# Performance work log

Measured on AMD Instinct MI355X. Metric: run time of the kernel, lower is better.

The kernel has to match this reference:

```python
import jax, jax.numpy as jnp
import numpy as np

N_TX, N_USER, N_MERCH = 100000, 20000, 5000
E = 400000
F_IN, H, L = 32, 256, 2


def setup_inputs() -> dict:
    key = jax.random.key(0)
    ks = jax.random.split(key, 24)
    p = lambda k, s: 0.02 * jax.random.normal(k, s, dtype=jnp.float32)
    return {
        "x_tx": jax.random.normal(ks[0], (N_TX, F_IN), dtype=jnp.float32),
        "x_user": jax.random.normal(ks[1], (N_USER, H), dtype=jnp.float32),
        "x_merch": jax.random.normal(ks[2], (N_MERCH, H), dtype=jnp.float32),
        # input projection
        "Wp": p(ks[3], (F_IN, H)), "bp": jnp.zeros((H,), jnp.float32),
        # per-layer, per-edge-type SAGEConv params: lin_l (neighbor, with bias) and lin_r (root, no bias)
        "Wl": p(ks[4], (L, 4, H, H)), "bl": jnp.zeros((L, 4, H), jnp.float32),
        "Wr": p(ks[5], (L, 4, H, H)),
        # classifier head
        "Wc1": p(ks[6], (H, H // 2)), "bc1": jnp.zeros((H // 2,), jnp.float32),
        "Wc2": p(ks[7], (H // 2, 1)), "bc2": jnp.zeros((1,), jnp.float32),
        # revenue head
        "Wv1": p(ks[8], (H, H // 2)), "bv1": jnp.zeros((H // 2,), jnp.float32),
        "Wv2": p(ks[9], (H // 2, 1)), "bv2": jnp.zeros((1,), jnp.float32),
        # edge lists (src, dst) per relation
        "e_ut_src": jax.random.randint(ks[10], (E,), 0, N_USER, dtype=jnp.int32),
        "e_ut_dst": jax.random.randint(ks[11], (E,), 0, N_TX, dtype=jnp.int32),
        "e_tm_src": jax.random.randint(ks[12], (E,), 0, N_TX, dtype=jnp.int32),
        "e_tm_dst": jax.random.randint(ks[13], (E,), 0, N_MERCH, dtype=jnp.int32),
        "e_mt_src": jax.random.randint(ks[14], (E,), 0, N_MERCH, dtype=jnp.int32),
        "e_mt_dst": jax.random.randint(ks[15], (E,), 0, N_TX, dtype=jnp.int32),
        "e_tu_src": jax.random.randint(ks[16], (E,), 0, N_TX, dtype=jnp.int32),
        "e_tu_dst": jax.random.randint(ks[17], (E,), 0, N_USER, dtype=jnp.int32),
    }


def _seg_mean(x_src, src, dst, n_dst):
    # gather source features per edge, scatter-mean into destinations
    msg = x_src[src]                                        # [E, H]
    s = jax.ops.segment_sum(msg, dst, num_segments=n_dst)   # [n_dst, H]
    cnt = jax.ops.segment_sum(jnp.ones((dst.shape[0],), x_src.dtype), dst, num_segments=n_dst)
    return s / jnp.maximum(cnt, 1.0)[:, None]


def _sage(x_src, x_dst, src, dst, Wl, bl, Wr):
    # PyG SAGEConv: lin_l(mean_neighbors) + lin_r(x_dst)
    m = _seg_mean(x_src, src, dst, x_dst.shape[0])
    return m @ Wl + bl + x_dst @ Wr


def reference(x_tx, x_user, x_merch, Wp, bp, Wl, bl, Wr,
              Wc1, bc1, Wc2, bc2, Wv1, bv1, Wv2, bv2,
              e_ut_src, e_ut_dst, e_tm_src, e_tm_dst,
              e_mt_src, e_mt_dst, e_tu_src, e_tu_dst):
    xt = x_tx @ Wp + bp          # input_proj on 'transaction'
    xu, xm = x_user, x_merch     # already hidden_dim -> used as-is
    for l in range(L):
        t_from_u = _sage(xu, xt, e_ut_src, e_ut_dst, Wl[l, 0], bl[l, 0], Wr[l, 0])
        m_from_t = _sage(xt, xm, e_tm_src, e_tm_dst, Wl[l, 1], bl[l, 1], Wr[l, 1])
        t_from_m = _sage(xm, xt, e_mt_src, e_mt_dst, Wl[l, 2], bl[l, 2], Wr[l, 2])
        u_from_t = _sage(xt, xu, e_tu_src, e_tu_dst, Wl[l, 3], bl[l, 3], Wr[l, 3])
        # HeteroConv aggr='mean' over edge types per destination, then ReLU (dropout = identity in eval)
        xt = jax.nn.relu(0.5 * (t_from_u + t_from_m))
        xm = jax.nn.relu(m_from_t)
        xu = jax.nn.relu(u_from_t)
    fraud_logits = (jax.nn.relu(xt @ Wc1 + bc1) @ Wc2 + bc2)[:, 0]
    revenue_pred = (jax.nn.relu(xt @ Wv1 + bv1) @ Wv2 + bv2)[:, 0]
    return fraud_logits, revenue_pred
```

## Files before the change

kernel.cpp:

```cpp
#include <hip/hip_runtime.h>

#define NTX 100000
#define NUSER 20000
#define NMERCH 5000
#define HD 256
#define ROWPAD 128

using u16 = unsigned short;
typedef __attribute__((ext_vector_type(8))) short bf16x8;
typedef __attribute__((ext_vector_type(4))) float f32x4;

__device__ __forceinline__ u16 f2bf(float f){
  unsigned u = __float_as_uint(f);
  unsigned r = (u + 0x7FFFu + ((u >> 16) & 1u)) >> 16;
  return (u16)r;
}
__device__ __forceinline__ float bf2f(u16 b){
  return __uint_as_float(((unsigned)b) << 16);
}
__device__ __forceinline__ unsigned pk2(float a, float b){
  return (unsigned)f2bf(a) | ((unsigned)f2bf(b) << 16);
}

__device__ __forceinline__ void gather4(const u16* __restrict__ T, const int* __restrict__ ss,
    int j0, int j1, int lane, int c, float& o0, float& o1, float& o2, float& o3){
  float a0=0,a1=0,a2=0,a3=0, b0=0,b1=0,b2=0,b3=0;
  float c0=0,c1=0,c2=0,c3=0, d0=0,d1=0,d2=0,d3=0;
  for (int base = j0; base < j1; base += 64){
    int n = j1 - base; if (n > 64) n = 64;
    int idx = ss[base + (lane < n ? lane : 0)];
    for (int jj = 0; jj < n; jj += 4){
      int s0 = __shfl(idx, jj);
      int s1 = __shfl(idx, jj+1);
      int s2 = __shfl(idx, jj+2);
      int s3 = __shfl(idx, jj+3);
      ushort4 v0 = *(const ushort4*)(T + (size_t)s0*HD + c);
      ushort4 v1 = *(const ushort4*)(T + (size_t)s1*HD + c);
      ushort4 v2 = *(const ushort4*)(T + (size_t)s2*HD + c);
      ushort4 v3 = *(const ushort4*)(T + (size_t)s3*HD + c);
      a0 += bf2f(v0.x); a1 += bf2f(v0.y); a2 += bf2f(v0.z); a3 += bf2f(v0.w);
      if (jj+1 < n){ b0 += bf2f(v1.x); b1 += bf2f(v1.y); b2 += bf2f(v1.z); b3 += bf2f(v1.w); }
      if (jj+2 < n){ c0 += bf2f(v2.x); c1 += bf2f(v2.y); c2 += bf2f(v2.z); c3 += bf2f(v2.w); }
      if (jj+3 < n){ d0 += bf2f(v3.x); d1 += bf2f(v3.y); d2 += bf2f(v3.z); d3 += bf2f(v3.w); }
    }
  }
  o0 += (a0+b0)+(c0+d0); o1 += (a1+b1)+(c1+d1);
  o2 += (a2+b2)+(c2+d2); o3 += (a3+b3)+(c3+d3);
}

__device__ __forceinline__ int rel_n(int y){ return y==0?NTX: y==1?NMERCH: y==2?NTX:NUSER; }
__device__ __forceinline__ int rel_coff(int y){ return y==0?0: y==1?100000: y==2?105000:205000; }
__device__ __forceinline__ int rel_rpoff(int y){ return y==0?0: y==1?100001: y==2?105002:205003; }
__device__ __forceinline__ int rel_shift(int y){ return y==0?11: y==1?8: y==2?11:10; }
__device__ __forceinline__ int rel_np(int y){ return y==0?49: y==1?20: y==2?49:20; }
#define ECH 128
#define PSTW 72

__global__ __launch_bounds__(256) void csrA_kernel(const int* __restrict__ d0p, const int* __restrict__ d1p,
    const int* __restrict__ d2p, const int* __restrict__ d3p, int nE, int* __restrict__ PC){
  int y = blockIdx.y;
  const int* dst = y==0?d0p: y==1?d1p: y==2?d2p:d3p;
  int shift = rel_shift(y);
  __shared__ int cc[64];
  int t = threadIdx.x;
  if (t < 64) cc[t] = 0;
  __syncthreads();
  int CH = (nE + ECH - 1)/ECH;
  int e0 = blockIdx.x*CH, e1 = e0 + CH; if (e1 > nE) e1 = nE;
  for (int e = e0 + t*4; e < e1; e += 1024){
    int a = dst[e];
    int b = (e+1 < e1) ? dst[e+1] : -1;
    int c = (e+2 < e1) ? dst[e+2] : -1;
    int d = (e+3 < e1) ? dst[e+3] : -1;
    atomicAdd(&cc[a>>shift], 1);
    if (b >= 0) atomicAdd(&cc[b>>shift], 1);
    if (c >= 0) atomicAdd(&cc[c>>shift], 1);
    if (d >= 0) atomicAdd(&cc[d>>shift], 1);
  }
  __syncthreads();
  if (t < 64) PC[(((size_t)y*ECH + blockIdx.x)<<6) + t] = cc[t];
}

__global__ void csrB_kernel(int* __restrict__ PC, int* __restrict__ PST, int* __restrict__ RP, int nE){
  int y = blockIdx.y;
  int np = rel_np(y);
  int t = threadIdx.x;
  __shared__ int sh[64];
  int run = 0;
  if (t < np){
    for (int c = 0; c < ECH; ++c){
      size_t idx = (((size_t)y*ECH + c)<<6) + t;
      int v = PC[idx]; PC[idx] = run; run += v;
    }
  }
  sh[t] = run;
  __syncthreads();
  if (t == 0){
    int acc = 0;
    for (int i = 0; i < np; ++i){ int v = sh[i]; sh[i] = acc; acc += v; }
    PST[y*PSTW + np] = nE;
    RP[rel_rpoff(y) + rel_n(y)] = nE;
  }
  __syncthreads();
  if (t < np){
    int base = sh[t];
    PST[y*PSTW + t] = base;
    for (int c = 0; c < ECH; ++c){
      size_t idx = (((size_t)y*ECH + c)<<6) + t;
      PC[idx] += base;
    }
  }
}

__global__ __launch_bounds__(256) void csrC_kernel(
    const int* __restrict__ s0p, const int* __restrict__ d0p,
    const int* __restrict__ s1p, const int* __restrict__ d1p,
    const int* __restrict__ s2p, const int* __restrict__ d2p,
    const int* __restrict__ s3p, const int* __restrict__ d3p,
    const int* __restrict__ PC, int* __restrict__ EB, int nE){
  int y = blockIdx.y;
  const int* src = y==0?s0p: y==1?s1p: y==2?s2p:s3p;
  const int* dst = y==0?d0p: y==1?d1p: y==2?d2p:d3p;
  int shift = rel_shift(y);
  int mask = (1<<shift) - 1;
  __shared__ int cur[64];
  int t = threadIdx.x;
  if (t < 64) cur[t] = PC[(((size_t)y*ECH + blockIdx.x)<<6) + t];
  __syncthreads();
  int CH = (nE + ECH - 1)/ECH;
  int e0 = blockIdx.x*CH, e1 = e0 + CH; if (e1 > nE) e1 = nE;
  int* eb = EB + (size_t)y*nE;
  for (int e = e0 + t*4; e < e1; e += 1024){
    #pragma unroll
    for (int u = 0; u < 4; ++u){
      int ee = e + u;
      if (ee < e1){
        int d = dst[ee], s = src[ee];
        int pos = atomicAdd(&cur[d>>shift], 1);
        eb[pos] = ((d & mask) << 17) | s;
      }
    }
  }
}

__global__ __launch_bounds__(256) void csrD_kernel(const int* __restrict__ EB, const int* __restrict__ PST,
    int* __restrict__ RP, float* __restrict__ INV,
    int* __restrict__ ss0, int* __restrict__ ss1, int* __restrict__ ss2, int* __restrict__ ss3, int nE){
  int y = blockIdx.y;
  int np = rel_np(y);
  int part = blockIdx.x;
  if (part >= np) return;
  int shift = rel_shift(y);
  int n = rel_n(y);
  int gbase = part << shift;
  int len = n - gbase; int range = 1 << shift; if (len > range) len = range;
  __shared__ int cnt[2048];
  __shared__ int curs[2048];
  __shared__ int sh[256];
  int t = threadIdx.x;
  for (int i = t; i < len; i += 256) cnt[i] = 0;
  __syncthreads();
  const int* eb = EB + (size_t)y*nE;
  int j0 = PST[y*PSTW + part], j1 = PST[y*PSTW + part + 1];
  for (int j = j0 + t*4; j < j1; j += 1024){
    int a = eb[j];
    int b = (j+1 < j1) ? eb[j+1] : -1;
    int c = (j+2 < j1) ? eb[j+2] : -1;
    int d = (j+3 < j1) ? eb[j+3] : -1;
    atomicAdd(&cnt[a>>17], 1);
    if (b >= 0) atomicAdd(&cnt[b>>17], 1);
    if (c >= 0) atomicAdd(&cnt[c>>17], 1);
    if (d >= 0) atomicAdd(&cnt[d>>17], 1);
  }
  __syncthreads();
  int base8 = t*8;
  int vals[8]; int tsum = 0;
  #pragma unroll
  for (int u = 0; u < 8; ++u){
    int i = base8 + u;
    int v = (i < len) ? cnt[i] : 0;
    vals[u] = tsum; tsum += v;
  }
  sh[t] = tsum;
  __syncthreads();
  for (int o = 1; o < 256; o <<= 1){
    int v = (t >= o) ? sh[t-o] : 0;
    __syncthreads();
    sh[t] += v;
    __syncthreads();
  }
  int tbase = j0 + sh[t] - tsum;
  int rpo = rel_rpoff(y) + gbase;
  int ivo = rel_coff(y) + gbase;
  #pragma unroll
  for (int u = 0; u < 8; ++u){
    int i = base8 + u;
    if (i < len){
      int start = tbase + vals[u];
      curs[i] = start;
      RP[rpo + i] = start;
      INV[ivo + i] = 1.f/fmaxf((float)cnt[i], 1.f);
    }
  }
  __syncthreads();
  int* ss = y==0?ss0: y==1?ss1: y==2?ss2:ss3;
  for (int j = j0 + t*4; j < j1; j += 1024){
    #pragma unroll
    for (int u = 0; u < 4; ++u){
      int jj = j + u;
      if (jj < j1){
        int pk = eb[jj];
        int pos = atomicAdd(&curs[pk>>17], 1);
        ss[pos] = pk & 0x1FFFF;
      }
    }
  }
}

__global__ __launch_bounds__(256) void wprep_kernel(const float* __restrict__ Wl, const float* __restrict__ Wr,
    const float* __restrict__ Wp, const float* __restrict__ Wc1, const float* __restrict__ Wv1,
    const float* __restrict__ bc1, const float* __restrict__ bv1,
    u16* __restrict__ WTl, u16* __restrict__ WTr1, u16* __restrict__ WTr3, u16* __restrict__ WT02,
    u16* __restrict__ WTH, u16* __restrict__ WTp, float* __restrict__ bH){
  int y = blockIdx.y;
  int i = blockIdx.x*256 + threadIdx.x;
  if (y < 8){
    if (i < 65536){ int k=i>>8, n=i&255; WTl[(size_t)y*65536 + n*256 + k] = f2bf(Wl[(size_t)y*65536 + i]); }
  } else if (y < 10){
    int l = y-8;
    if (i < 65536){ int k=i>>8, n=i&255; WTr1[(size_t)l*65536 + n*256 + k] = f2bf(Wr[(size_t)(l*4+1)*65536 + i]); }
  } else if (y < 12){
    int l = y-10;
    if (i < 65536){ int k=i>>8, n=i&255; WTr3[(size_t)l*65536 + n*256 + k] = f2bf(Wr[(size_t)(l*4+3)*65536 + i]); }
  } else if (y < 14){
    int l = y-12;
    if (i < 65536){ int k=i>>8, n=i&255;
      WT02[(size_t)l*65536 + n*256 + k] = f2bf(Wr[(size_t)(l*4+0)*65536 + i] + Wr[(size_t)(l*4+2)*65536 + i]); }
  } else if (y == 14){
    if (i < 65536){ int k=i>>8, n=i&255;
      float v = (n < 128) ? Wc1[k*128 + n] : Wv1[k*128 + (n-128)];
      WTH[(size_t)n*256 + k] = f2bf(v); }
  } else {
    if (i < 8192){ int k=i>>8, n=i&255; WTp[(size_t)n*32 + k] = f2bf(Wp[i]); }
    if (i < 256) bH[i] = (i < 128) ? bc1[i] : bv1[i-128];
  }
}

__global__ __launch_bounds__(256) void cvt2_kernel(const float* __restrict__ xu,
    const float* __restrict__ xm, u16* __restrict__ XU, u16* __restrict__ XM){
  int y = blockIdx.y;
  const float* in = y==0?xu:xm;
  u16* out = y==0?XU:XM;
  int n4 = y==0?NUSER*HD/4:NMERCH*HD/4;
  int i = blockIdx.x*256 + threadIdx.x;
  if (i >= n4) return;
  float4 v = ((const float4*)in)[i];
  ushort4 o; o.x = f2bf(v.x); o.y = f2bf(v.y); o.z = f2bf(v.z); o.w = f2bf(v.w);
  ((ushort4*)out)[i] = o;
}

__global__ __launch_bounds__(256) void proj_gemm_kernel(const float* __restrict__ A, const u16* __restrict__ WT,
    const float* __restrict__ bias, u16* __restrict__ C, int M){
  __shared__ u16 As[128][40];
  __shared__ u16 Bs[128][40];
  int m0 = blockIdx.x * 128, n0 = blockIdx.y * 128;
  int t = threadIdx.x;
  int w = t >> 6, lane = t & 63;
  int wm = (w >> 1) << 6, wn = (w & 1) << 6;
  int lm = lane & 15;
  int lk = (lane >> 4) << 3;
  int sr = t >> 1, sc = (t & 1) << 4;
  float4 f0 = {0,0,0,0}, f1 = {0,0,0,0}, f2 = {0,0,0,0}, f3 = {0,0,0,0};
  if (m0 + sr < M){
    const float* ap = A + (size_t)(m0+sr)*32 + sc;
    f0 = *(const float4*)(ap+0); f1 = *(const float4*)(ap+4);
    f2 = *(const float4*)(ap+8); f3 = *(const float4*)(ap+12);
  }
  uint4 q0, q1;
  q0.x = pk2(f0.x,f0.y); q0.y = pk2(f0.z,f0.w); q0.z = pk2(f1.x,f1.y); q0.w = pk2(f1.z,f1.w);
  q1.x = pk2(f2.x,f2.y); q1.y = pk2(f2.z,f2.w); q1.z = pk2(f3.x,f3.y); q1.w = pk2(f3.z,f3.w);
  *(uint4*)&As[sr][sc] = q0;
  *(uint4*)&As[sr][sc+8] = q1;
  const u16* bp_ = WT + (size_t)(n0+sr)*32 + sc;
  *(uint4*)&Bs[sr][sc]   = *(const uint4*)(bp_);
  *(uint4*)&Bs[sr][sc+8] = *(const uint4*)(bp_ + 8);
  __syncthreads();
  bf16x8 af[4], bf[4];
  #pragma unroll
  for (int i = 0; i < 4; ++i) af[i] = *(const bf16x8*)&As[wm + i*16 + lm][lk];
  #pragma unroll
  for (int j = 0; j < 4; ++j) bf[j] = *(const bf16x8*)&Bs[wn + j*16 + lm][lk];
  f32x4 acc[4][4] = {};
  #pragma unroll
  for (int i = 0; i < 4; ++i)
    #pragma unroll
    for (int j = 0; j < 4; ++j)
      acc[i][j] = __builtin_amdgcn_mfma_f32_16x16x32_bf16(af[i], bf[j], acc[i][j], 0, 0, 0);
  int rsub = (lane >> 4) << 2;
  #pragma unroll
  for (int j = 0; j < 4; ++j){
    int col = n0 + wn + j*16 + lm;
    float bv = bias[col];
    #pragma unroll
    for (int i = 0; i < 4; ++i){
      int rbase = m0 + wm + i*16 + rsub;
      #pragma unroll
      for (int r = 0; r < 4; ++r){
        int row = rbase + r;
        if (row < M) C[(size_t)row*HD + col] = f2bf(acc[i][j][r] + bv);
      }
    }
  }
}

template<bool CBF, bool BIAS, bool RELU, bool ACCUM>
__global__ __launch_bounds__(256) void mfma_gemm_kernel(const u16* __restrict__ A, const u16* __restrict__ BT,
    const float* __restrict__ bias, const float* __restrict__ Cadd, void* __restrict__ Cp, int M, int K, int N){
  __shared__ u16 As[128][40];
  __shared__ u16 Bs[128][40];
  int m0 = blockIdx.x * 128, n0 = blockIdx.y * 128;
  int t = threadIdx.x;
  int w = t >> 6, lane = t & 63;
  int wm = (w >> 1) << 6, wn = (w & 1) << 6;
  int lm = lane & 15;
  int lk = (lane >> 4) << 3;
  f32x4 acc[4][4] = {};
  int sr0 = t >> 2, sk0 = (t & 3) << 3;
  int sr1 = sr0 + 64;
  for (int k0 = 0; k0 < K; k0 += 32){
    uint4 a0 = *(const uint4*)(A  + (size_t)(m0+sr0)*K + k0 + sk0);
    uint4 a1 = *(const uint4*)(A  + (size_t)(m0+sr1)*K + k0 + sk0);
    uint4 b0 = *(const uint4*)(BT + (size_t)(n0+sr0)*K + k0 + sk0);
    uint4 b1 = *(const uint4*)(BT + (size_t)(n0+sr1)*K + k0 + sk0);
    *(uint4*)&As[sr0][sk0] = a0;
    *(uint4*)&As[sr1][sk0] = a1;
    *(uint4*)&Bs[sr0][sk0] = b0;
    *(uint4*)&Bs[sr1][sk0] = b1;
    __syncthreads();
    bf16x8 af[4], bf[4];
    #pragma unroll
    for (int i = 0; i < 4; ++i) af[i] = *(const bf16x8*)&As[wm + i*16 + lm][lk];
    #pragma unroll
    for (int j = 0; j < 4; ++j) bf[j] = *(const bf16x8*)&Bs[wn + j*16 + lm][lk];
    #pragma unroll
    for (int i = 0; i < 4; ++i)
      #pragma unroll
      for (int j = 0; j < 4; ++j)
        acc[i][j] = __builtin_amdgcn_mfma_f32_16x16x32_bf16(af[i], bf[j], acc[i][j], 0, 0, 0);
    __syncthreads();
  }
  int rsub = (lane >> 4) << 2;
  #pragma unroll
  for (int j = 0; j < 4; ++j){
    int col = n0 + wn + j*16 + lm;
    float bv = 0.f;
    if constexpr (BIAS) bv = bias[col];
    #pragma unroll
    for (int i = 0; i < 4; ++i){
      int rbase = m0 + wm + i*16 + rsub;
      #pragma unroll
      for (int r = 0; r < 4; ++r){
        int row = rbase + r;
        if (row < M){
          float v = acc[i][j][r] + bv;
          if constexpr (ACCUM) v += Cadd[(size_t)row*N + col];
          if constexpr (RELU) v = fmaxf(v, 0.f);
          if constexpr (CBF) ((u16*)Cp)[(size_t)row*N + col] = f2bf(v);
          else               ((float*)Cp)[(size_t)row*N + col] = v;
        }
      }
    }
  }
}

__global__ __launch_bounds__(256) void pair_gemm_kernel(
    const u16* __restrict__ A0, const u16* __restrict__ W0, u16* __restrict__ C0, int M0,
    const u16* __restrict__ A1, const u16* __restrict__ W1, u16* __restrict__ C1, int M1){
  int z = blockIdx.z;
  const u16* A = z ? A1 : A0;
  const u16* WT = z ? W1 : W0;
  u16* C = z ? C1 : C0;
  int M = z ? M1 : M0;
  int m0 = blockIdx.x * 128, n0 = blockIdx.y * 128;
  if (m0 >= M) return;
  __shared__ u16 As[128][40];
  __shared__ u16 Bs[128][40];
  int t = threadIdx.x;
  int w = t >> 6, lane = t & 63;
  int wm = (w >> 1) << 6, wn = (w & 1) << 6;
  int lm = lane & 15;
  int lk = (lane >> 4) << 3;
  f32x4 acc[4][4] = {};
  int sr0 = t >> 2, sk0 = (t & 3) << 3;
  int sr1 = sr0 + 64;
  for (int k0 = 0; k0 < 256; k0 += 32){
    uint4 a0 = *(const uint4*)(A  + (size_t)(m0+sr0)*256 + k0 + sk0);
    uint4 a1 = *(const uint4*)(A  + (size_t)(m0+sr1)*256 + k0 + sk0);
    uint4 b0 = *(const uint4*)(WT + (size_t)(n0+sr0)*256 + k0 + sk0);
    uint4 b1 = *(const uint4*)(WT + (size_t)(n0+sr1)*256 + k0 + sk0);
    *(uint4*)&As[sr0][sk0] = a0;
    *(uint4*)&As[sr1][sk0] = a1;
    *(uint4*)&Bs[sr0][sk0] = b0;
    *(uint4*)&Bs[sr1][sk0] = b1;
    __syncthreads();
    bf16x8 af[4], bf[4];
    #pragma unroll
    for (int i = 0; i < 4; ++i) af[i] = *(const bf16x8*)&As[wm + i*16 + lm][lk];
    #pragma unroll
    for (int j = 0; j < 4; ++j) bf[j] = *(const bf16x8*)&Bs[wn + j*16 + lm][lk];
    #pragma unroll
    for (int i = 0; i < 4; ++i)
      #pragma unroll
      for (int j = 0; j < 4; ++j)
        acc[i][j] = __builtin_amdgcn_mfma_f32_16x16x32_bf16(af[i], bf[j], acc[i][j], 0, 0, 0);
    __syncthreads();
  }
  int rsub = (lane >> 4) << 2;
  #pragma unroll
  for (int j = 0; j < 4; ++j){
    int col = n0 + wn + j*16 + lm;
    #pragma unroll
    for (int i = 0; i < 4; ++i){
      int rbase = m0 + wm + i*16 + rsub;
      #pragma unroll
      for (int r = 0; r < 4; ++r){
        int row = rbase + r;
        if (row < M) C[(size_t)row*256 + col] = f2bf(acc[i][j][r]);
      }
    }
  }
}

__global__ __launch_bounds__(256) void pair_gemm2_kernel(
    const u16* __restrict__ G0, const u16* __restrict__ X0, const u16* __restrict__ Wa0, const u16* __restrict__ Wb0,
    const float* __restrict__ b0, u16* __restrict__ C0, int M0,
    const u16* __restrict__ G1, const u16* __restrict__ X1, const u16* __restrict__ Wa1, const u16* __restrict__ Wb1,
    const float* __restrict__ b1, u16* __restrict__ C1, int M1){
  int z = blockIdx.z;
  const u16* G  = z ? G1 : G0;
  const u16* X  = z ? X1 : X0;
  const u16* Wa = z ? Wa1 : Wa0;
  const u16* Wb = z ? Wb1 : Wb0;
  const float* bias = z ? b1 : b0;
  u16* C = z ? C1 : C0;
  int M = z ? M1 : M0;
  int m0 = blockIdx.x * 128, n0 = blockIdx.y * 128;
  if (m0 >= M) return;
  __shared__ u16 As[128][40];
  __shared__ u16 Bs[128][40];
  int t = threadIdx.x;
  int w = t >> 6, lane = t & 63;
  int wm = (w >> 1) << 6, wn = (w & 1) << 6;
  int lm = lane & 15;
  int lk = (lane >> 4) << 3;
  f32x4 acc[4][4] = {};
  int sr0 = t >> 2, sk0 = (t & 3) << 3;
  int sr1 = sr0 + 64;
  for (int k0 = 0; k0 < 512; k0 += 32){
    const u16* A  = (k0 < 256) ? G : X;
    const u16* WT = (k0 < 256) ? Wa : Wb;
    int kk = k0 & 255;
    uint4 a0 = *(const uint4*)(A  + (size_t)(m0+sr0)*256 + kk + sk0);
    uint4 a1 = *(const uint4*)(A  + (size_t)(m0+sr1)*256 + kk + sk0);
    uint4 b0_ = *(const uint4*)(WT + (size_t)(n0+sr0)*256 + kk + sk0);
    uint4 b1_ = *(const uint4*)(WT + (size_t)(n0+sr1)*256 + kk + sk0);
    *(uint4*)&As[sr0][sk0] = a0;
    *(uint4*)&As[sr1][sk0] = a1;
    *(uint4*)&Bs[sr0][sk0] = b0_;
    *(uint4*)&Bs[sr1][sk0] = b1_;
    __syncthreads();
    bf16x8 af[4], bf[4];
    #pragma unroll
    for (int i = 0; i < 4; ++i) af[i] = *(const bf16x8*)&As[wm + i*16 + lm][lk];
    #pragma unroll
    for (int j = 0; j < 4; ++j) bf[j] = *(const bf16x8*)&Bs[wn + j*16 + lm][lk];
    #pragma unroll
    for (int i = 0; i < 4; ++i)
      #pragma unroll
      for (int j = 0; j < 4; ++j)
        acc[i][j] = __builtin_amdgcn_mfma_f32_16x16x32_bf16(af[i], bf[j], acc[i][j], 0, 0, 0);
    __syncthreads();
  }
  int rsub = (lane >> 4) << 2;
  #pragma unroll
  for (int j = 0; j < 4; ++j){
    int col = n0 + wn + j*16 + lm;
    float bv = bias[col];
    #pragma unroll
    for (int i = 0; i < 4; ++i){
      int rbase = m0 + wm + i*16 + rsub;
      #pragma unroll
      for (int r = 0; r < 4; ++r){
        int row = rbase + r;
        if (row < M) C[(size_t)row*256 + col] = f2bf(fmaxf(acc[i][j][r] + bv, 0.f));
      }
    }
  }
}

__global__ __launch_bounds__(256) void gather_pair_kernel(const u16* __restrict__ XT,
    const int* __restrict__ rp0, const int* __restrict__ ss0, const float* __restrict__ inv0,
    u16* __restrict__ out0, int M0,
    const int* __restrict__ rp1, const int* __restrict__ ss1, const float* __restrict__ inv1,
    u16* __restrict__ out1, int M1){
  int y = blockIdx.y;
  const int* rp = y ? rp1 : rp0;
  const int* ss = y ? ss1 : ss0;
  const float* inv = y ? inv1 : inv0;
  u16* out = y ? out1 : out0;
  int M = y ? M1 : M0;
  int d = blockIdx.x*4 + (threadIdx.x >> 6);
  if (d >= M) return;
  int lane = threadIdx.x & 63;
  int c = lane << 2;
  float o0=0,o1=0,o2=0,o3=0;
  gather4(XT, ss, rp[d], rp[d+1], lane, c, o0, o1, o2, o3);
  float sc = inv[d];
  ushort4 o; o.x = f2bf(o0*sc); o.y = f2bf(o1*sc); o.z = f2bf(o2*sc); o.w = f2bf(o3*sc);
  *(ushort4*)(out + (size_t)d*HD + c) = o;
}

__global__ __launch_bounds__(256) void fused_tx_kernel(const u16* __restrict__ ACCb,
    const u16* __restrict__ Tu, const u16* __restrict__ Tm,
    const int* __restrict__ rpu, const int* __restrict__ ssu, const float* __restrict__ invu,
    const int* __restrict__ rpm, const int* __restrict__ ssm, const float* __restrict__ invm,
    const float* __restrict__ b0, const float* __restrict__ b2, u16* __restrict__ XT, int M){
  int d = blockIdx.x*4 + (threadIdx.x >> 6);
  if (d >= M) return;
  int lane = threadIdx.x & 63;
  int c = lane << 2;
  ushort4 av = *(const ushort4*)(ACCb + (size_t)d*HD + c);
  float r0 = bf2f(av.x), r1 = bf2f(av.y), r2 = bf2f(av.z), r3 = bf2f(av.w);
  {
    float s0=0,s1=0,s2=0,s3=0;
    gather4(Tu, ssu, rpu[d], rpu[d+1], lane, c, s0, s1, s2, s3);
    float sc = invu[d];
    r0 += s0*sc; r1 += s1*sc; r2 += s2*sc; r3 += s3*sc;
  }
  {
    float s0=0,s1=0,s2=0,s3=0;
    gather4(Tm, ssm, rpm[d], rpm[d+1], lane, c, s0, s1, s2, s3);
    float sc = invm[d];
    r0 += s0*sc; r1 += s1*sc; r2 += s2*sc; r3 += s3*sc;
  }
  float4 bb0 = *(const float4*)(b0 + c);
  float4 bb2 = *(const float4*)(b2 + c);
  ushort4 o;
  o.x = f2bf(fmaxf(0.5f*(r0 + bb0.x + bb2.x), 0.f));
  o.y = f2bf(fmaxf(0.5f*(r1 + bb0.y + bb2.y), 0.f));
  o.z = f2bf(fmaxf(0.5f*(r2 + bb0.z + bb2.z), 0.f));
  o.w = f2bf(fmaxf(0.5f*(r3 + bb0.w + bb2.w), 0.f));
  *(ushort4*)(XT + (size_t)d*HD + c) = o;
}

__global__ __launch_bounds__(256) void fused_head_kernel(const u16* __restrict__ A, const u16* __restrict__ BT,
    const float* __restrict__ bias, const float* __restrict__ Wc2, const float* __restrict__ bc2,
    const float* __restrict__ Wv2, const float* __restrict__ bv2, float* __restrict__ out, int M){
  __shared__ u16 As[128][40];
  __shared__ u16 Bs[128][40];
  __shared__ float hpart[128];
  int m0 = blockIdx.x * 128, n0 = blockIdx.y * 128;
  int t = threadIdx.x;
  int w = t >> 6, lane = t & 63;
  int wm = (w >> 1) << 6, wn = (w & 1) << 6;
  int lm = lane & 15;
  int lk = (lane >> 4) << 3;
  if (t < 128) hpart[t] = 0.f;
  f32x4 acc[4][4] = {};
  int sr0 = t >> 2, sk0 = (t & 3) << 3;
  int sr1 = sr0 + 64;
  for (int k0 = 0; k0 < 256; k0 += 32){
    uint4 a0 = *(const uint4*)(A  + (size_t)(m0+sr0)*256 + k0 + sk0);
    uint4 a1 = *(const uint4*)(A  + (size_t)(m0+sr1)*256 + k0 + sk0);
    uint4 b0 = *(const uint4*)(BT + (size_t)(n0+sr0)*256 + k0 + sk0);
    uint4 b1 = *(const uint4*)(BT + (size_t)(n0+sr1)*256 + k0 + sk0);
    *(uint4*)&As[sr0][sk0] = a0;
    *(uint4*)&As[sr1][sk0] = a1;
    *(uint4*)&Bs[sr0][sk0] = b0;
    *(uint4*)&Bs[sr1][sk0] = b1;
    __syncthreads();
    bf16x8 af[4], bf[4];
    #pragma unroll
    for (int i = 0; i < 4; ++i) af[i] = *(const bf16x8*)&As[wm + i*16 + lm][lk];
    #pragma unroll
    for (int j = 0; j < 4; ++j) bf[j] = *(const bf16x8*)&Bs[wn + j*16 + lm][lk];
    #pragma unroll
    for (int i = 0; i < 4; ++i)
      #pragma unroll
      for (int j = 0; j < 4; ++j)
        acc[i][j] = __builtin_amdgcn_mfma_f32_16x16x32_bf16(af[i], bf[j], acc[i][j], 0, 0, 0);
    __syncthreads();
  }
  const float* w2 = blockIdx.y ? Wv2 : Wc2;
  float badd = blockIdx.y ? bv2[0] : bc2[0];
  size_t outoff = blockIdx.y ? (size_t)M : 0;
  int rsub = (lane >> 4) << 2;
  float w2v[4], bv[4];
  #pragma unroll
  for (int j = 0; j < 4; ++j){
    w2v[j] = w2[wn + j*16 + lm];
    bv[j]  = bias[n0 + wn + j*16 + lm];
  }
  #pragma unroll
  for (int i = 0; i < 4; ++i){
    #pragma unroll
    for (int r = 0; r < 4; ++r){
      float p = 0.f;
      #pragma unroll
      for (int j = 0; j < 4; ++j) p += fmaxf(acc[i][j][r] + bv[j], 0.f) * w2v[j];
      p += __shfl_xor(p, 1); p += __shfl_xor(p, 2);
      p += __shfl_xor(p, 4); p += __shfl_xor(p, 8);
      if (lm == 0) atomicAdd(&hpart[wm + i*16 + rsub + r], p);
    }
  }
  __syncthreads();
  if (t < 128){
    int row = m0 + t;
    if (row < M) out[outoff + row] = hpart[t] + badd;
  }
}

extern "C" void kernel_launch(void* const* d_in, const int* in_sizes, int n_in,
                              void* d_out, int out_size, void* d_ws, size_t ws_size,
                              hipStream_t stream){
  const float* x_tx   = (const float*)d_in[0];
  const float* x_user = (const float*)d_in[1];
  const float* x_merch= (const float*)d_in[2];
  const float* Wp  = (const float*)d_in[3];
  const float* bp  = (const float*)d_in[4];
  const float* Wl  = (const float*)d_in[5];
  const float* bl  = (const float*)d_in[6];
  const float* Wr  = (const float*)d_in[7];
  const float* Wc1 = (const float*)d_in[8];
  const float* bc1 = (const float*)d_in[9];
  const float* Wc2 = (const float*)d_in[10];
  const float* bc2 = (const float*)d_in[11];
  const float* Wv1 = (const float*)d_in[12];
  const float* bv1 = (const float*)d_in[13];
  const float* Wv2 = (const float*)d_in[14];
  const float* bv2 = (const float*)d_in[15];
  const int* e_ut_s = (const int*)d_in[16];
  const int* e_ut_d = (const int*)d_in[17];
  const int* e_tm_s = (const int*)d_in[18];
  const int* e_tm_d = (const int*)d_in[19];
  const int* e_mt_s = (const int*)d_in[20];
  const int* e_mt_d = (const int*)d_in[21];
  const int* e_tu_s = (const int*)d_in[22];
  const int* e_tu_d = (const int*)d_in[23];
  float* out = (float*)d_out;
  const int NE = in_sizes[16];

  char* p = (char*)d_ws;
  auto take = [&](size_t bytes)->char*{ char* r = p; p += (bytes + 255) & ~(size_t)255; return r; };
  u16*   XT    = (u16*)  take((size_t)(NTX+ROWPAD)*HD*2);
  u16*   ACCb  = (u16*)  take((size_t)(NTX+ROWPAD)*HD*2);
  u16*   Tu    = (u16*)  take((size_t)NUSER*HD*2);
  u16*   Tm    = (u16*)  take((size_t)NMERCH*HD*2);
  u16*   AGGU  = (u16*)  take((size_t)(NUSER+ROWPAD)*HD*2);
  u16*   AGGM  = (u16*)  take((size_t)(NMERCH+ROWPAD)*HD*2);
  u16*   XU0   = (u16*)  take((size_t)(NUSER+ROWPAD)*HD*2);
  u16*   XU1   = (u16*)  take((size_t)(NUSER+ROWPAD)*HD*2);
  u16*   XM0   = (u16*)  take((size_t)(NMERCH+ROWPAD)*HD*2);
  u16*   XM1   = (u16*)  take((size_t)(NMERCH+ROWPAD)*HD*2);
  float* INV   = (float*)take((size_t)225000*4);
  int*   RP    = (int*)  take((size_t)225008*4);
  int*   SS_ut = (int*)  take((size_t)NE*4);
  int*   SS_tm = (int*)  take((size_t)NE*4);
  int*   SS_mt = (int*)  take((size_t)NE*4);
  int*   SS_tu = (int*)  take((size_t)NE*4);
  int*   PC    = (int*)  take((size_t)4*ECH*64*4);
  int*   PST   = (int*)  take((size_t)4*PSTW*4);
  int*   EB    = (int*)  take((size_t)4*NE*4);
  u16*   WTp   = (u16*)  take((size_t)32*256*2);
  u16*   WTl   = (u16*)  take((size_t)8*65536*2);
  u16*   WTr1  = (u16*)  take((size_t)2*65536*2);
  u16*   WTr3  = (u16*)  take((size_t)2*65536*2);
  u16*   WT02  = (u16*)  take((size_t)2*65536*2);
  u16*   WTH   = (u16*)  take((size_t)65536*2);
  float* bH    = (float*)take((size_t)256*4);

  float* inv_ut = INV,  *inv_tm = INV+100000, *inv_mt = INV+105000, *inv_tu = INV+205000;
  int*   rp_ut  = RP,   *rp_tm  = RP+100001,  *rp_mt  = RP+105002,  *rp_tu  = RP+205003;

  csrA_kernel<<<dim3(ECH,4),256,0,stream>>>(e_ut_d, e_tm_d, e_mt_d, e_tu_d, NE, PC);
  csrB_kernel<<<dim3(1,4),64,0,stream>>>(PC, PST, RP, NE);
  csrC_kernel<<<dim3(ECH,4),256,0,stream>>>(e_ut_s, e_ut_d, e_tm_s, e_tm_d, e_mt_s, e_mt_d,
      e_tu_s, e_tu_d, PC, EB, NE);
  csrD_kernel<<<dim3(49,4),256,0,stream>>>(EB, PST, RP, INV, SS_ut, SS_tm, SS_mt, SS_tu, NE);

  wprep_kernel<<<dim3(256,16),256,0,stream>>>(Wl, Wr, Wp, Wc1, Wv1, bc1, bv1,
      WTl, WTr1, WTr3, WT02, WTH, WTp, bH);

  cvt2_kernel<<<dim3(5000,2),256,0,stream>>>(x_user, x_merch, XU0, XM0);
  proj_gemm_kernel<<<dim3(782,2),256,0,stream>>>(x_tx, WTp, bp, XT, NTX);

  u16* xu_cur = XU0; u16* xu_nxt = XU1;
  u16* xm_cur = XM0; u16* xm_nxt = XM1;

  for (int l = 0; l < 2; ++l){
    const float* bl_l = bl + (size_t)l*4*256;
    u16* WTl_l = WTl + (size_t)l*4*65536;

    gather_pair_kernel<<<dim3(5000,2),256,0,stream>>>(XT,
        rp_tm, SS_tm, inv_tm, AGGM, NMERCH,
        rp_tu, SS_tu, inv_tu, AGGU, NUSER);

    pair_gemm_kernel<<<dim3(157,2,2),256,0,stream>>>(
        xu_cur, WTl_l + 0*65536, Tu, NUSER,
        xm_cur, WTl_l + 2*65536, Tm, NMERCH);

    mfma_gemm_kernel<true,false,false,false><<<dim3(782,2),256,0,stream>>>(
        XT, WT02 + (size_t)l*65536, nullptr, nullptr, ACCb, NTX, 256, 256);
    fused_tx_kernel<<<(NTX+3)/4,256,0,stream>>>(ACCb, Tu, Tm,
        rp_ut, SS_ut, inv_ut, rp_mt, SS_mt, inv_mt,
        bl_l + 0*256, bl_l + 2*256, XT, NTX);

    pair_gemm2_kernel<<<dim3(157,2,2),256,0,stream>>>(
        AGGU, xu_cur, WTl_l + 3*65536, WTr3 + (size_t)l*65536, bl_l + 3*256, xu_nxt, NUSER,
        AGGM, xm_cur, WTl_l + 1*65536, WTr1 + (size_t)l*65536, bl_l + 1*256, xm_nxt, NMERCH);

    { u16* tmp = xu_cur; xu_cur = xu_nxt; xu_nxt = tmp; }
    { u16* tmp = xm_cur; xm_cur = xm_nxt; xm_nxt = tmp; }
  }

  fused_head_kernel<<<dim3(782,2),256,0,stream>>>(XT, WTH, bH, Wc2, bc2, Wv2, bv2, out, NTX);
}
```

Before: 541.3 us.

## Horizontally fuse per-layer GEMMs and gathers into two block-partitioned mega kernels

Each layer's four launches (gather pair, neighbor pair GEMM, transaction root GEMM, fused tx aggregation, plus pair_gemm2) become two kernels. Each kernel splits its 1-D grid by block index across independent GEMM tiles and gather/aggregation rows. The aim is to cut launch gaps and tail idling from the small user/merchant GEMMs, and to let those overlap with the memory-bound gathers. In exchange, every block now statically allocates 20KB of LDS, including gather-only blocks, which may limit occupancy for the gather and aggregation work.

```diff
diff --git a/kernel.cpp b/kernel.cpp
--- a/kernel.cpp
+++ b/kernel.cpp
@@ -313,78 +313,8 @@
   }
 }
 
-template<bool CBF, bool BIAS, bool RELU, bool ACCUM>
-__global__ __launch_bounds__(256) void mfma_gemm_kernel(const u16* __restrict__ A, const u16* __restrict__ BT,
-    const float* __restrict__ bias, const float* __restrict__ Cadd, void* __restrict__ Cp, int M, int K, int N){
-  __shared__ u16 As[128][40];
-  __shared__ u16 Bs[128][40];
-  int m0 = blockIdx.x * 128, n0 = blockIdx.y * 128;
-  int t = threadIdx.x;
-  int w = t >> 6, lane = t & 63;
-  int wm = (w >> 1) << 6, wn = (w & 1) << 6;
-  int lm = lane & 15;
-  int lk = (lane >> 4) << 3;
-  f32x4 acc[4][4] = {};
-  int sr0 = t >> 2, sk0 = (t & 3) << 3;
-  int sr1 = sr0 + 64;
-  for (int k0 = 0; k0 < K; k0 += 32){
-    uint4 a0 = *(const uint4*)(A  + (size_t)(m0+sr0)*K + k0 + sk0);
-    uint4 a1 = *(const uint4*)(A  + (size_t)(m0+sr1)*K + k0 + sk0);
-    uint4 b0 = *(const uint4*)(BT + (size_t)(n0+sr0)*K + k0 + sk0);
-    uint4 b1 = *(const uint4*)(BT + (size_t)(n0+sr1)*K + k0 + sk0);
-    *(uint4*)&As[sr0][sk0] = a0;
-    *(uint4*)&As[sr1][sk0] = a1;
-    *(uint4*)&Bs[sr0][sk0] = b0;
-    *(uint4*)&Bs[sr1][sk0] = b1;
-    __syncthreads();
-    bf16x8 af[4], bf[4];
-    #pragma unroll
-    for (int i = 0; i < 4; ++i) af[i] = *(const bf16x8*)&As[wm + i*16 + lm][lk];
-    #pragma unroll
-    for (int j = 0; j < 4; ++j) bf[j] = *(const bf16x8*)&Bs[wn + j*16 + lm][lk];
-    #pragma unroll
-    for (int i = 0; i < 4; ++i)
-      #pragma unroll
-      for (int j = 0; j < 4; ++j)
-        acc[i][j] = __builtin_amdgcn_mfma_f32_16x16x32_bf16(af[i], bf[j], acc[i][j], 0, 0, 0);
-    __syncthreads();
-  }
-  int rsub = (lane >> 4) << 2;
-  #pragma unroll
-  for (int j = 0; j < 4; ++j){
-    int col = n0 + wn + j*16 + lm;
-    float bv = 0.f;
-    if constexpr (BIAS) bv = bias[col];
-    #pragma unroll
-    for (int i = 0; i < 4; ++i){
-      int rbase = m0 + wm + i*16 + rsub;
-      #pragma unroll
-      for (int r = 0; r < 4; ++r){
-        int row = rbase + r;
-        if (row < M){
-          float v = acc[i][j][r] + bv;
-          if constexpr (ACCUM) v += Cadd[(size_t)row*N + col];
-          if constexpr (RELU) v = fmaxf(v, 0.f);
-          if constexpr (CBF) ((u16*)Cp)[(size_t)row*N + col] = f2bf(v);
-          else               ((float*)Cp)[(size_t)row*N + col] = v;
-        }
-      }
-    }
-  }
-}
-
-__global__ __launch_bounds__(256) void pair_gemm_kernel(
-    const u16* __restrict__ A0, const u16* __restrict__ W0, u16* __restrict__ C0, int M0,
-    const u16* __restrict__ A1, const u16* __restrict__ W1, u16* __restrict__ C1, int M1){
-  int z = blockIdx.z;
-  const u16* A = z ? A1 : A0;
-  const u16* WT = z ? W1 : W0;
-  u16* C = z ? C1 : C0;
-  int M = z ? M1 : M0;
-  int m0 = blockIdx.x * 128, n0 = blockIdx.y * 128;
-  if (m0 >= M) return;
-  __shared__ u16 As[128][40];
-  __shared__ u16 Bs[128][40];
+__device__ __forceinline__ void gemm_nb_body(const u16* __restrict__ A, const u16* __restrict__ WT,
+    u16* __restrict__ C, int M, int m0, int n0, u16* As, u16* Bs){
   int t = threadIdx.x;
   int w = t >> 6, lane = t & 63;
   int wm = (w >> 1) << 6, wn = (w & 1) << 6;
@@ -398,16 +328,16 @@
     uint4 a1 = *(const uint4*)(A  + (size_t)(m0+sr1)*256 + k0 + sk0);
     uint4 b0 = *(const uint4*)(WT + (size_t)(n0+sr0)*256 + k0 + sk0);
     uint4 b1 = *(const uint4*)(WT + (size_t)(n0+sr1)*256 + k0 + sk0);
-    *(uint4*)&As[sr0][sk0] = a0;
-    *(uint4*)&As[sr1][sk0] = a1;
-    *(uint4*)&Bs[sr0][sk0] = b0;
-    *(uint4*)&Bs[sr1][sk0] = b1;
+    *(uint4*)&As[sr0*40 + sk0] = a0;
+    *(uint4*)&As[sr1*40 + sk0] = a1;
+    *(uint4*)&Bs[sr0*40 + sk0] = b0;
+    *(uint4*)&Bs[sr1*40 + sk0] = b1;
     __syncthreads();
     bf16x8 af[4], bf[4];
     #pragma unroll
-    for (int i = 0; i < 4; ++i) af[i] = *(const bf16x8*)&As[wm + i*16 + lm][lk];
-    #pragma unroll
-    for (int j = 0; j < 4; ++j) bf[j] = *(const bf16x8*)&Bs[wn + j*16 + lm][lk];
+    for (int i = 0; i < 4; ++i) af[i] = *(const bf16x8*)&As[(wm + i*16 + lm)*40 + lk];
+    #pragma unroll
+    for (int j = 0; j < 4; ++j) bf[j] = *(const bf16x8*)&Bs[(wn + j*16 + lm)*40 + lk];
     #pragma unroll
     for (int i = 0; i < 4; ++i)
       #pragma unroll
@@ -431,23 +361,9 @@
   }
 }
 
-__global__ __launch_bounds__(256) void pair_gemm2_kernel(
-    const u16* __restrict__ G0, const u16* __restrict__ X0, const u16* __restrict__ Wa0, const u16* __restrict__ Wb0,
-    const float* __restrict__ b0, u16* __restrict__ C0, int M0,
-    const u16* __restrict__ G1, const u16* __restrict__ X1, const u16* __restrict__ Wa1, const u16* __restrict__ Wb1,
-    const float* __restrict__ b1, u16* __restrict__ C1, int M1){
-  int z = blockIdx.z;
-  const u16* G  = z ? G1 : G0;
-  const u16* X  = z ? X1 : X0;
-  const u16* Wa = z ? Wa1 : Wa0;
-  const u16* Wb = z ? Wb1 : Wb0;
-  const float* bias = z ? b1 : b0;
-  u16* C = z ? C1 : C0;
-  int M = z ? M1 : M0;
-  int m0 = blockIdx.x * 128, n0 = blockIdx.y * 128;
-  if (m0 >= M) return;
-  __shared__ u16 As[128][40];
-  __shared__ u16 Bs[128][40];
+__device__ __forceinline__ void gemm2_body(const u16* __restrict__ G, const u16* __restrict__ X,
+    const u16* __restrict__ Wa, const u16* __restrict__ Wb, const float* __restrict__ bias,
+    u16* __restrict__ C, int M, int m0, int n0, u16* As, u16* Bs){
   int t = threadIdx.x;
   int w = t >> 6, lane = t & 63;
   int wm = (w >> 1) << 6, wn = (w & 1) << 6;
@@ -464,16 +380,16 @@
     uint4 a1 = *(const uint4*)(A  + (size_t)(m0+sr1)*256 + kk + sk0);
     uint4 b0_ = *(const uint4*)(WT + (size_t)(n0+sr0)*256 + kk + sk0);
     uint4 b1_ = *(const uint4*)(WT + (size_t)(n0+sr1)*256 + kk + sk0);
-    *(uint4*)&As[sr0][sk0] = a0;
-    *(uint4*)&As[sr1][sk0] = a1;
-    *(uint4*)&Bs[sr0][sk0] = b0_;
-    *(uint4*)&Bs[sr1][sk0] = b1_;
+    *(uint4*)&As[sr0*40 + sk0] = a0;
+    *(uint4*)&As[sr1*40 + sk0] = a1;
+    *(uint4*)&Bs[sr0*40 + sk0] = b0_;
+    *(uint4*)&Bs[sr1*40 + sk0] = b1_;
     __syncthreads();
     bf16x8 af[4], bf[4];
     #pragma unroll
-    for (int i = 0; i < 4; ++i) af[i] = *(const bf16x8*)&As[wm + i*16 + lm][lk];
-    #pragma unroll
-    for (int j = 0; j < 4; ++j) bf[j] = *(const bf16x8*)&Bs[wn + j*16 + lm][lk];
+    for (int i = 0; i < 4; ++i) af[i] = *(const bf16x8*)&As[(wm + i*16 + lm)*40 + lk];
+    #pragma unroll
+    for (int j = 0; j < 4; ++j) bf[j] = *(const bf16x8*)&Bs[(wn + j*16 + lm)*40 + lk];
     #pragma unroll
     for (int i = 0; i < 4; ++i)
       #pragma unroll
@@ -498,18 +414,10 @@
   }
 }
 
-__global__ __launch_bounds__(256) void gather_pair_kernel(const u16* __restrict__ XT,
-    const int* __restrict__ rp0, const int* __restrict__ ss0, const float* __restrict__ inv0,
-    u16* __restrict__ out0, int M0,
-    const int* __restrict__ rp1, const int* __restrict__ ss1, const float* __restrict__ inv1,
-    u16* __restrict__ out1, int M1){
-  int y = blockIdx.y;
-  const int* rp = y ? rp1 : rp0;
-  const int* ss = y ? ss1 : ss0;
-  const float* inv = y ? inv1 : inv0;
-  u16* out = y ? out1 : out0;
-  int M = y ? M1 : M0;
-  int d = blockIdx.x*4 + (threadIdx.x >> 6);
+__device__ __forceinline__ void gather_body(const u16* __restrict__ XT,
+    const int* __restrict__ rp, const int* __restrict__ ss, const float* __restrict__ inv,
+    u16* __restrict__ out, int M, int bx){
+  int d = bx*4 + (threadIdx.x >> 6);
   if (d >= M) return;
   int lane = threadIdx.x & 63;
   int c = lane << 2;
@@ -520,12 +428,12 @@
   *(ushort4*)(out + (size_t)d*HD + c) = o;
 }
 
-__global__ __launch_bounds__(256) void fused_tx_kernel(const u16* __restrict__ ACCb,
+__device__ __forceinline__ void fused_tx_body(const u16* __restrict__ ACCb,
     const u16* __restrict__ Tu, const u16* __restrict__ Tm,
     const int* __restrict__ rpu, const int* __restrict__ ssu, const float* __restrict__ invu,
     const int* __restrict__ rpm, const int* __restrict__ ssm, const float* __restrict__ invm,
-    const float* __restrict__ b0, const float* __restrict__ b2, u16* __restrict__ XT, int M){
-  int d = blockIdx.x*4 + (threadIdx.x >> 6);
+    const float* __restrict__ b0, const float* __restrict__ b2, u16* __restrict__ XT, int M, int bx){
+  int d = bx*4 + (threadIdx.x >> 6);
   if (d >= M) return;
   int lane = threadIdx.x & 63;
   int c = lane << 2;
@@ -551,6 +459,58 @@
   o.z = f2bf(fmaxf(0.5f*(r2 + bb0.z + bb2.z), 0.f));
   o.w = f2bf(fmaxf(0.5f*(r3 + bb0.w + bb2.w), 0.f));
   *(ushort4*)(XT + (size_t)d*HD + c) = o;
+}
+
+__global__ __launch_bounds__(256) void megaA_kernel(
+    const u16* __restrict__ XT, const u16* __restrict__ WT02l, u16* __restrict__ ACCb,
+    const u16* __restrict__ xu, const u16* __restrict__ Wl0, u16* __restrict__ Tu,
+    const u16* __restrict__ xm, const u16* __restrict__ Wl2, u16* __restrict__ Tm,
+    const int* __restrict__ rp_tm, const int* __restrict__ ss_tm, const float* __restrict__ inv_tm, u16* __restrict__ AGGM,
+    const int* __restrict__ rp_tu, const int* __restrict__ ss_tu, const float* __restrict__ inv_tu, u16* __restrict__ AGGU){
+  __shared__ u16 smem[10240];
+  int b = blockIdx.x;
+  if (b < 1564){
+    int ny = (b >= 782) ? 1 : 0;
+    int x = b - ny*782;
+    gemm_nb_body(XT, WT02l, ACCb, NTX, x*128, ny*128, smem, smem + 5120);
+  } else if (b < 1958){
+    int bb = b - 1564;
+    if (bb < 314){
+      int ny = bb / 157, x = bb - ny*157;
+      gemm_nb_body(xu, Wl0, Tu, NUSER, x*128, ny*128, smem, smem + 5120);
+    } else {
+      bb -= 314;
+      int ny = bb / 40, x = bb - ny*40;
+      gemm_nb_body(xm, Wl2, Tm, NMERCH, x*128, ny*128, smem, smem + 5120);
+    }
+  } else if (b < 3208){
+    gather_body(XT, rp_tm, ss_tm, inv_tm, AGGM, NMERCH, b - 1958);
+  } else {
+    gather_body(XT, rp_tu, ss_tu, inv_tu, AGGU, NUSER, b - 3208);
+  }
+}
+
+__global__ __launch_bounds__(256) void megaB_kernel(
+    const u16* __restrict__ AGGU, const u16* __restrict__ xu, const u16* __restrict__ Wa3,
+    const u16* __restrict__ Wb3, const float* __restrict__ b3, u16* __restrict__ xu_nxt,
+    const u16* __restrict__ AGGM, const u16* __restrict__ xm, const u16* __restrict__ Wa1,
+    const u16* __restrict__ Wb1, const float* __restrict__ b1, u16* __restrict__ xm_nxt,
+    const u16* __restrict__ ACCb, const u16* __restrict__ Tu, const u16* __restrict__ Tm,
+    const int* __restrict__ rpu, const int* __restrict__ ssu, const float* __restrict__ invu,
+    const int* __restrict__ rpm, const int* __restrict__ ssm, const float* __restrict__ invm,
+    const float* __restrict__ bb0, const float* __restrict__ bb2, u16* __restrict__ XT){
+  __shared__ u16 smem[10240];
+  int b = blockIdx.x;
+  if (b < 314){
+    int ny = b / 157, x = b - ny*157;
+    gemm2_body(AGGU, xu, Wa3, Wb3, b3, xu_nxt, NUSER, x*128, ny*128, smem, smem + 5120);
+  } else if (b < 394){
+    int bb = b - 314;
+    int ny = bb / 40, x = bb - ny*40;
+    gemm2_body(AGGM, xm, Wa1, Wb1, b1, xm_nxt, NMERCH, x*128, ny*128, smem, smem + 5120);
+  } else {
+    fused_tx_body(ACCb, Tu, Tm, rpu, ssu, invu, rpm, ssm, invm, bb0, bb2, XT, NTX, b - 394);
+  }
 }
 
 __global__ __launch_bounds__(256) void fused_head_kernel(const u16* __restrict__ A, const u16* __restrict__ BT,
@@ -701,23 +661,19 @@
     const float* bl_l = bl + (size_t)l*4*256;
     u16* WTl_l = WTl + (size_t)l*4*65536;
 
-    gather_pair_kernel<<<dim3(5000,2),256,0,stream>>>(XT,
-        rp_tm, SS_tm, inv_tm, AGGM, NMERCH,
-        rp_tu, SS_tu, inv_tu, AGGU, NUSER);
-
-    pair_gemm_kernel<<<dim3(157,2,2),256,0,stream>>>(
-        xu_cur, WTl_l + 0*65536, Tu, NUSER,
-        xm_cur, WTl_l + 2*65536, Tm, NMERCH);
-
-    mfma_gemm_kernel<true,false,false,false><<<dim3(782,2),256,0,stream>>>(
-        XT, WT02 + (size_t)l*65536, nullptr, nullptr, ACCb, NTX, 256, 256);
-    fused_tx_kernel<<<(NTX+3)/4,256,0,stream>>>(ACCb, Tu, Tm,
+    megaA_kernel<<<8208,256,0,stream>>>(
+        XT, WT02 + (size_t)l*65536, ACCb,
+        xu_cur, WTl_l + 0*65536, Tu,
+        xm_cur, WTl_l + 2*65536, Tm,
+        rp_tm, SS_tm, inv_tm, AGGM,
+        rp_tu, SS_tu, inv_tu, AGGU);
+
+    megaB_kernel<<<25394,256,0,stream>>>(
+        AGGU, xu_cur, WTl_l + 3*65536, WTr3 + (size_t)l*65536, bl_l + 3*256, xu_nxt,
+        AGGM, xm_cur, WTl_l + 1*65536, WTr1 + (size_t)l*65536, bl_l + 1*256, xm_nxt,
+        ACCb, Tu, Tm,
         rp_ut, SS_ut, inv_ut, rp_mt, SS_mt, inv_mt,
-        bl_l + 0*256, bl_l + 2*256, XT, NTX);
-
-    pair_gemm2_kernel<<<dim3(157,2,2),256,0,stream>>>(
-        AGGU, xu_cur, WTl_l + 3*65536, WTr3 + (size_t)l*65536, bl_l + 3*256, xu_nxt, NUSER,
-        AGGM, xm_cur, WTl_l + 1*65536, WTr1 + (size_t)l*65536, bl_l + 1*256, xm_nxt, NMERCH);
+        bl_l + 0*256, bl_l + 2*256, XT);
 
     { u16* tmp = xu_cur; xu_cur = xu_nxt; xu_nxt = tmp; }
     { u16* tmp = xm_cur; xm_cur = xm_nxt; xm_nxt = tmp; }
```

Measured after the change: 643.9 us (median of 2 runs). +19.0%, slower.
